# Kernel tuning notes

Hardware: AMD Instinct MI355X
Metric: run time of the kernel (lower is better)

The kernel has to match this reference:

```python
import jax, jax.numpy as jnp
import numpy as np

EMBED_DIM = 1024
NUM_HEADS = 16
HEAD_DIM = EMBED_DIM // NUM_HEADS
B, T = 4, 2048


def setup_inputs() -> dict:
    key = jax.random.key(0)
    ks = jax.random.split(key, 5)
    s = 1.0 / np.sqrt(EMBED_DIM)
    x = jax.random.normal(ks[0], (B, T, EMBED_DIM), dtype=jnp.float32)
    attention_mask = jnp.ones((B, 1, 1, T), dtype=jnp.int32)
    # torch Linear weights: qkv (3E, E), out (E, E); store transposed for x @ W
    W_qkv = jax.random.uniform(ks[1], (EMBED_DIM, 3 * EMBED_DIM), jnp.float32, -s, s)
    b_qkv = jax.random.uniform(ks[2], (3 * EMBED_DIM,), jnp.float32, -s, s)
    W_out = jax.random.uniform(ks[3], (EMBED_DIM, EMBED_DIM), jnp.float32, -s, s)
    b_out = jax.random.uniform(ks[4], (EMBED_DIM,), jnp.float32, -s, s)
    return {"x": x, "attention_mask": attention_mask,
            "W_qkv": W_qkv, "b_qkv": b_qkv, "W_out": W_out, "b_out": b_out}


def reference(x, attention_mask, W_qkv, b_qkv, W_out, b_out):
    Bq, Tq, E = x.shape
    qkv = x @ W_qkv + b_qkv                              # [B,T,3E]
    qkv = qkv.reshape(Bq, Tq, 3, NUM_HEADS, HEAD_DIM)
    qkv = jnp.transpose(qkv, (2, 0, 3, 1, 4))            # [3,B,H,T,d]
    q, k, v = qkv[0], qkv[1], qkv[2]
    scores = jnp.einsum('bhqd,bhkd->bhqk', q, k) / jnp.sqrt(
        jnp.asarray(HEAD_DIM, x.dtype))                  # [B,H,T,T]
    scores = jnp.where(attention_mask == 0, jnp.asarray(-jnp.inf, x.dtype), scores)
    attn = jax.nn.softmax(scores, axis=-1)
    ctx = jnp.einsum('bhqk,bhkd->bhqd', attn, v)         # [B,H,T,d]
    ctx = jnp.transpose(ctx, (0, 2, 1, 3)).reshape(Bq, Tq, E)
    return ctx @ W_out + b_out
```

## Files before the change

### kernel.cpp

```cpp
#include <hip/hip_runtime.h>
#include <hip/hip_bf16.h>
#include <stdint.h>


typedef __attribute__((ext_vector_type(8))) short short8;
typedef __attribute__((ext_vector_type(4))) float f32x4;
typedef __attribute__((ext_vector_type(16))) float f32x16;
typedef __attribute__((ext_vector_type(4))) unsigned short ushort4_t;
typedef __attribute__((ext_vector_type(8))) unsigned short ushort8_t;

#define SEQ 2048
#define EDIM 1024
#define QSCALE 0.18033688011112042f

__device__ __forceinline__ unsigned short f2bf(float x) {
  union { float f; uint32_t u; } v; v.f = x;
  uint32_t r = v.u + 0x7fffu + ((v.u >> 16) & 1u);
  return (unsigned short)(r >> 16);
}

__device__ __forceinline__ uint32_t cvtpk(float lo, float hi) {
  uint32_t r;
  asm("v_cvt_pk_bf16_f32 %0, %1, %2" : "=v"(r) : "v"(lo), "v"(hi));
  return r;
}

__device__ __forceinline__ float exp2_raw(float x) {
  float r;
  asm("v_exp_f32 %0, %1" : "=v"(r) : "v"(x));
  return r;
}

__device__ __forceinline__ void gload_lds16(const void* g, void* l) {
  typedef __attribute__((address_space(1))) const unsigned int gu32;
  typedef __attribute__((address_space(3))) unsigned int lu32;
  __builtin_amdgcn_global_load_lds((gu32*)g, (lu32*)l, 16, 0, 0);
}

__global__ void k_prep(const float* __restrict__ x,
                       unsigned short* __restrict__ xb,
                       const float* __restrict__ Wq,
                       unsigned short* __restrict__ wqt,
                       const float* __restrict__ Wo,
                       unsigned short* __restrict__ wot) {
  __shared__ float tile[32][33];
  const int id = blockIdx.x;
  if (id < 4096) {
    const int i = id * 256 + threadIdx.x;
    const float4* p = ((const float4*)x) + (size_t)i * 2;
    float4 a = p[0], b = p[1];
    ushort8_t v;
    v[0] = f2bf(a.x); v[1] = f2bf(a.y); v[2] = f2bf(a.z); v[3] = f2bf(a.w);
    v[4] = f2bf(b.x); v[5] = f2bf(b.y); v[6] = f2bf(b.z); v[7] = f2bf(b.w);
    ((ushort8_t*)xb)[i] = v;
    return;
  }
  const float* W;
  unsigned short* Wt;
  int N, bx, by;
  if (id < 7168) { W = Wq; Wt = wqt; N = 3072; bx = (id - 4096) % 96; by = (id - 4096) / 96; }
  else           { W = Wo; Wt = wot; N = 1024; bx = (id - 7168) % 32; by = (id - 7168) / 32; }
  const int K = 1024;
  const int c0 = bx * 32, r0 = by * 32;
  const int tx = threadIdx.x & 31, ty = threadIdx.x >> 5;
#pragma unroll
  for (int i = 0; i < 4; ++i) {
    int r = ty + i * 8;
    tile[r][tx] = W[(size_t)(r0 + r) * N + c0 + tx];
  }
  __syncthreads();
#pragma unroll
  for (int i = 0; i < 4; ++i) {
    int r = ty + i * 8;
    Wt[(size_t)(c0 + r) * K + r0 + tx] = f2bf(tile[tx][r]);
  }
}

template <int EPI, int NBX>
__global__ __launch_bounds__(256, 2) void k_gemm(
    const unsigned short* __restrict__ A, const unsigned short* __restrict__ Bt,
    const float* __restrict__ bias, unsigned short* __restrict__ Qo,
    unsigned short* __restrict__ Ko, unsigned short* __restrict__ VTo,
    float* __restrict__ Out) {
  __shared__ unsigned short As[128 * 32];
  __shared__ unsigned short Bs[128 * 32];
  const int tid = threadIdx.x;
  const int lane = tid & 63, wid = tid >> 6;
  const int wr = wid >> 1, wc = wid & 1;
  const int g = lane >> 4, r = lane & 15;
  const int lid = blockIdx.y * NBX + blockIdx.x;
  const int total = NBX * gridDim.y;
  const int id = (lid & 7) * (total >> 3) + (lid >> 3);
  const int m0 = (id / NBX) * 128, n0 = (id % NBX) * 128;

  f32x4 zero4 = {0.f, 0.f, 0.f, 0.f};
  f32x4 acc[4][4];
#pragma unroll
  for (int mi = 0; mi < 4; ++mi)
#pragma unroll
    for (int ni = 0; ni < 4; ++ni) acc[mi][ni] = zero4;

  for (int kt = 0; kt < 1024; kt += 32) {
#pragma unroll
    for (int i = 0; i < 2; ++i) {
      int seg = i * 256 + tid;
      int row = seg >> 2, sl = seg & 3;
      gload_lds16(A + (size_t)(m0 + row) * 1024 + kt + sl * 8,
                  (char*)As + (i * 256 + wid * 64) * 16);
      gload_lds16(Bt + (size_t)(n0 + row) * 1024 + kt + sl * 8,
                  (char*)Bs + (i * 256 + wid * 64) * 16);
    }
    __syncthreads();
    short8 af[4], bf[4];
#pragma unroll
    for (int mi = 0; mi < 4; ++mi)
      af[mi] = *(const short8*)&As[(wr * 64 + mi * 16 + r) * 32 + g * 8];
#pragma unroll
    for (int ni = 0; ni < 4; ++ni)
      bf[ni] = *(const short8*)&Bs[(wc * 64 + ni * 16 + r) * 32 + g * 8];
#pragma unroll
    for (int mi = 0; mi < 4; ++mi)
#pragma unroll
      for (int ni = 0; ni < 4; ++ni)
        acc[mi][ni] = __builtin_amdgcn_mfma_f32_16x16x32_bf16(
            af[mi], bf[ni], acc[mi][ni], 0, 0, 0);
    __syncthreads();
  }

#pragma unroll
  for (int mi = 0; mi < 4; ++mi) {
#pragma unroll
    for (int ni = 0; ni < 4; ++ni) {
      const int n = n0 + wc * 64 + ni * 16 + r;
      const float bv = bias[n];
      const int mbase = m0 + wr * 64 + mi * 16 + g * 4;
      if (EPI == 0) {
        const int sec = n >> 10, e = n & 1023, h = e >> 6, dd = e & 63;
        const int b = mbase >> 11, t = mbase & 2047;
        if (sec == 2) {
          ushort4_t pk;
#pragma unroll
          for (int j = 0; j < 4; ++j) pk[j] = f2bf(acc[mi][ni][j] + bv);
          *(ushort4_t*)&VTo[(((size_t)b * 16 + h) * 64 + dd) * 2048 + t] = pk;
        } else {
          unsigned short* dst = (sec == 0) ? Qo : Ko;
          const float scl = (sec == 0) ? QSCALE : 1.0f;
#pragma unroll
          for (int j = 0; j < 4; ++j)
            dst[(((size_t)b * 16 + h) * 2048 + t + j) * 64 + dd] =
                f2bf((acc[mi][ni][j] + bv) * scl);
        }
      } else {
#pragma unroll
        for (int j = 0; j < 4; ++j)
          Out[(size_t)(mbase + j) * 1024 + n] = acc[mi][ni][j] + bv;
      }
    }
  }
}

__global__ __launch_bounds__(512, 4) void k_attn(
    const unsigned short* __restrict__ Qg, const unsigned short* __restrict__ Kg,
    const unsigned short* __restrict__ VTg, const int* __restrict__ maskp,
    unsigned short* __restrict__ ctx) {
  __shared__ unsigned short Ks[2][64 * 64];
  __shared__ unsigned short Vs[2][64 * 64];
  const int tid = threadIdx.x, lane = tid & 63, wid = tid >> 6;
  const int q = lane & 31, hi = lane >> 5;
  const int id = blockIdx.x;
  const int slot = id >> 3;
  const int bh = (id & 7) * 8 + (slot >> 3);
  const int b = bh >> 4, h = bh & 15;
  const int q0 = (slot & 7) * 256 + wid * 32;
  const int qr = q0 + q;

  const unsigned short* Qb = Qg + (size_t)bh * SEQ * 64;
  const unsigned short* Kb = Kg + (size_t)bh * SEQ * 64;
  const unsigned short* Vb = VTg + (size_t)bh * 64 * SEQ;
  const int* mb = maskp + b * SEQ;

  const int r0_ = tid >> 3, sl0_ = (tid & 7) ^ (r0_ & 7);
  const unsigned short* kp0 = Kb + r0_ * 64 + sl0_ * 8;
  const unsigned short* vp0 = Vb + (size_t)r0_ * SEQ + sl0_ * 8;
  char* kbase = (char*)Ks[0] + wid * 1024;
  char* vbase = (char*)Vs[0] + wid * 1024;

  auto STAGE = [&](int buf) {
    const int bo = buf * 8192;
    gload_lds16(kp0, kbase + bo);
    gload_lds16(vp0, vbase + bo);
    kp0 += 64 * 64;
    vp0 += 64;
  };

  short8 qf[4];
#pragma unroll
  for (int ds = 0; ds < 4; ++ds)
    qf[ds] = *(const short8*)&Qb[(size_t)qr * 64 + ds * 16 + hi * 8];

  short8 onesf;
#pragma unroll
  for (int j = 0; j < 8; ++j) onesf[j] = (short)0x3F80;

  f32x16 z16 = {0.f,0.f,0.f,0.f,0.f,0.f,0.f,0.f,0.f,0.f,0.f,0.f,0.f,0.f,0.f,0.f};
  f32x16 o0 = z16, o1 = z16;
  f32x16 osum = z16;
  const int kb4 = hi * 4;

  STAGE(0);
  const int* mptr = mb + lane;
  int mv = mptr[0];
  mptr += 64;

  for (int t = 0; t < 32; ++t) {
    const int cur = t & 1;
    __syncthreads();
    int mvn = 1;
    if (t < 31) {
      STAGE(cur ^ 1);
      mvn = mptr[0];
      mptr += 64;
    }
    const unsigned long long bits = __ballot(mv != 0);
    mv = mvn;

    const char* KsB = (const char*)Ks[cur];
    const char* VsB = (const char*)Vs[cur];
    f32x16 c0 = z16, c1 = z16;
    __builtin_amdgcn_s_setprio(1);
#pragma unroll
    for (int ds = 0; ds < 4; ++ds) {
      const int sl = ds * 2 + hi;
      short8 ka0 = *(const short8*)(KsB + q * 128 + ((sl ^ (q & 7)) * 16));
      short8 ka1 = *(const short8*)(KsB + (32 + q) * 128 + ((sl ^ (q & 7)) * 16));
      c0 = __builtin_amdgcn_mfma_f32_32x32x16_bf16(ka0, qf[ds], c0, 0, 0, 0);
      c1 = __builtin_amdgcn_mfma_f32_32x32x16_bf16(ka1, qf[ds], c1, 0, 0, 0);
    }
    __builtin_amdgcn_s_setprio(0);

#pragma unroll
    for (int i = 0; i < 16; ++i) {
      c0[i] = exp2_raw(c0[i]);
      c1[i] = exp2_raw(c1[i]);
    }
    if (bits != ~0ull) {
#pragma unroll
      for (int i = 0; i < 16; ++i) {
        const int k0 = (i & 3) + 8 * (i >> 2) + kb4;
        if (!((bits >> k0) & 1)) c0[i] = 0.f;
        if (!((bits >> (k0 + 32)) & 1)) c1[i] = 0.f;
      }
    }

    short8 pf[4];
#pragma unroll
    for (int sub = 0; sub < 2; ++sub) {
      uint32_t w[8];
#pragma unroll
      for (int j = 0; j < 8; ++j)
        w[j] = sub ? cvtpk(c1[2 * j], c1[2 * j + 1])
                   : cvtpk(c0[2 * j], c0[2 * j + 1]);
      asm("v_permlane32_swap_b32 %0, %1" : "+v"(w[0]), "+v"(w[2]));
      asm("v_permlane32_swap_b32 %0, %1" : "+v"(w[1]), "+v"(w[3]));
      asm("v_permlane32_swap_b32 %0, %1" : "+v"(w[4]), "+v"(w[6]));
      asm("v_permlane32_swap_b32 %0, %1" : "+v"(w[5]), "+v"(w[7]));
      union { uint32_t u[4]; short8 s; } ua, ub;
      ua.u[0] = w[0]; ua.u[1] = w[1]; ua.u[2] = w[2]; ua.u[3] = w[3];
      ub.u[0] = w[4]; ub.u[1] = w[5]; ub.u[2] = w[6]; ub.u[3] = w[7];
      pf[sub * 2] = ua.s;
      pf[sub * 2 + 1] = ub.s;
    }

    __builtin_amdgcn_s_setprio(1);
#pragma unroll
    for (int ks = 0; ks < 4; ++ks) {
      const int sl = ks * 2 + hi;
      short8 va0 = *(const short8*)(VsB + q * 128 + ((sl ^ (q & 7)) * 16));
      short8 va1 = *(const short8*)(VsB + (32 + q) * 128 + ((sl ^ (q & 7)) * 16));
      o0 = __builtin_amdgcn_mfma_f32_32x32x16_bf16(va0, pf[ks], o0, 0, 0, 0);
      o1 = __builtin_amdgcn_mfma_f32_32x32x16_bf16(va1, pf[ks], o1, 0, 0, 0);
      osum = __builtin_amdgcn_mfma_f32_32x32x16_bf16(onesf, pf[ks], osum,
                                                     0, 0, 0);
    }
    __builtin_amdgcn_s_setprio(0);
  }

  const float inv = 1.f / osum[0];
#pragma unroll
  for (int ns = 0; ns < 2; ++ns) {
#pragma unroll
    for (int g_ = 0; g_ < 4; ++g_) {
      ushort4_t v4;
#pragma unroll
      for (int e = 0; e < 4; ++e) {
        const float val = (ns ? o1[g_ * 4 + e] : o0[g_ * 4 + e]) * inv;
        v4[e] = f2bf(val);
      }
      *(ushort4_t*)&ctx[((size_t)b * SEQ + qr) * 1024 + h * 64 + ns * 32 +
                        g_ * 8 + hi * 4] = v4;
    }
  }
}

extern "C" void kernel_launch(void* const* d_in, const int* in_sizes, int n_in,
                              void* d_out, int out_size, void* d_ws,
                              size_t ws_size, hipStream_t stream) {
  const float* x = (const float*)d_in[0];
  const int* mask = (const int*)d_in[1];
  const float* Wqkv = (const float*)d_in[2];
  const float* bqkv = (const float*)d_in[3];
  const float* Wout = (const float*)d_in[4];
  const float* bout = (const float*)d_in[5];
  float* out = (float*)d_out;

  unsigned short* ws = (unsigned short*)d_ws;
  unsigned short* xb = ws;
  unsigned short* wqt = ws + 8388608;
  unsigned short* wot = ws + 11534336;
  unsigned short* Q = ws + 12582912;
  unsigned short* K = ws + 20971520;
  unsigned short* VT = ws + 29360128;
  unsigned short* ctx = xb;

  k_prep<<<8192, 256, 0, stream>>>(x, xb, Wqkv, wqt, Wout, wot);
  k_gemm<0, 24><<<dim3(24, 64), 256, 0, stream>>>(xb, wqt, bqkv, Q, K, VT,
                                                  nullptr);
  k_attn<<<512, 512, 0, stream>>>(Q, K, VT, mask, ctx);
  k_gemm<1, 8><<<dim3(8, 64), 256, 0, stream>>>(ctx, wot, bout, nullptr,
                                                nullptr, nullptr, out);
}
```

Measured before the change: 199.3 us.

## Double-buffer GEMM LDS tiles to overlap global loads with MFMA

Splits the A and B shared-memory tiles into two buffers. The next K-slice is issued to global-to-LDS loads before the current slice's MFMAs run, and each iteration needs only one barrier instead of two. Load addresses are precomputed as incrementing pointers. This hides global memory latency behind compute, at the cost of twice the LDS per block, which may reduce occupancy.

```diff
diff --git a/kernel.cpp b/kernel.cpp
--- a/kernel.cpp
+++ b/kernel.cpp
@@ -82,8 +82,8 @@
     const float* __restrict__ bias, unsigned short* __restrict__ Qo,
     unsigned short* __restrict__ Ko, unsigned short* __restrict__ VTo,
     float* __restrict__ Out) {
-  __shared__ unsigned short As[128 * 32];
-  __shared__ unsigned short Bs[128 * 32];
+  __shared__ unsigned short As[2][128 * 32];
+  __shared__ unsigned short Bs[2][128 * 32];
   const int tid = threadIdx.x;
   const int lane = tid & 63, wid = tid >> 6;
   const int wr = wid >> 1, wc = wid & 1;
@@ -93,6 +93,22 @@
   const int id = (lid & 7) * (total >> 3) + (lid >> 3);
   const int m0 = (id / NBX) * 128, n0 = (id % NBX) * 128;
 
+  const int row0 = tid >> 2, sl0 = tid & 3;
+  const unsigned short* a0 = A + (size_t)(m0 + row0) * 1024 + sl0 * 8;
+  const unsigned short* a1 = A + (size_t)(m0 + 64 + row0) * 1024 + sl0 * 8;
+  const unsigned short* b0 = Bt + (size_t)(n0 + row0) * 1024 + sl0 * 8;
+  const unsigned short* b1 = Bt + (size_t)(n0 + 64 + row0) * 1024 + sl0 * 8;
+  char* adst = (char*)As[0] + wid * 64 * 16;
+  char* bdst = (char*)Bs[0] + wid * 64 * 16;
+
+  auto STAGE = [&](int buf) {
+    const int bo = buf * 8192;
+    gload_lds16(a0, adst + bo);        a0 += 32;
+    gload_lds16(a1, adst + bo + 4096); a1 += 32;
+    gload_lds16(b0, bdst + bo);        b0 += 32;
+    gload_lds16(b1, bdst + bo + 4096); b1 += 32;
+  };
+
   f32x4 zero4 = {0.f, 0.f, 0.f, 0.f};
   f32x4 acc[4][4];
 #pragma unroll
@@ -100,31 +116,28 @@
 #pragma unroll
     for (int ni = 0; ni < 4; ++ni) acc[mi][ni] = zero4;
 
-  for (int kt = 0; kt < 1024; kt += 32) {
-#pragma unroll
-    for (int i = 0; i < 2; ++i) {
-      int seg = i * 256 + tid;
-      int row = seg >> 2, sl = seg & 3;
-      gload_lds16(A + (size_t)(m0 + row) * 1024 + kt + sl * 8,
-                  (char*)As + (i * 256 + wid * 64) * 16);
-      gload_lds16(Bt + (size_t)(n0 + row) * 1024 + kt + sl * 8,
-                  (char*)Bs + (i * 256 + wid * 64) * 16);
-    }
-    __syncthreads();
+  STAGE(0);
+  asm volatile("s_waitcnt vmcnt(0)" ::: "memory");
+  __builtin_amdgcn_s_barrier();
+
+  for (int t = 0; t < 32; ++t) {
+    const int cur = t & 1;
+    if (t < 31) STAGE(cur ^ 1);
     short8 af[4], bf[4];
 #pragma unroll
     for (int mi = 0; mi < 4; ++mi)
-      af[mi] = *(const short8*)&As[(wr * 64 + mi * 16 + r) * 32 + g * 8];
+      af[mi] = *(const short8*)&As[cur][(wr * 64 + mi * 16 + r) * 32 + g * 8];
 #pragma unroll
     for (int ni = 0; ni < 4; ++ni)
-      bf[ni] = *(const short8*)&Bs[(wc * 64 + ni * 16 + r) * 32 + g * 8];
+      bf[ni] = *(const short8*)&Bs[cur][(wc * 64 + ni * 16 + r) * 32 + g * 8];
 #pragma unroll
     for (int mi = 0; mi < 4; ++mi)
 #pragma unroll
       for (int ni = 0; ni < 4; ++ni)
         acc[mi][ni] = __builtin_amdgcn_mfma_f32_16x16x32_bf16(
             af[mi], bf[ni], acc[mi][ni], 0, 0, 0);
-    __syncthreads();
+    asm volatile("s_waitcnt vmcnt(0)" ::: "memory");
+    __builtin_amdgcn_s_barrier();
   }
 
 #pragma unroll
```

Result: no change. 198.2 us (-0.6%).
